# Kernel tuning notes

Hardware: AMD Instinct MI355X
Metric: run time of the kernel (lower is better)

The kernel has to match this reference:

```python
import jax, jax.numpy as jnp
import numpy as np


def _kernelize(data, projection_matrix):
    # FAVOR+ positive softmax features: ratio * h(x) * f(x @ P^T)
    # h(x) = exp(-||x||^2 / 2), f(u) = exp(u)
    d = data.shape[-1]
    r = projection_matrix.shape[0]
    data_norm = (d ** -0.25) * data                       # [n, d]
    ratio = r ** -0.5
    data_dash = jnp.einsum('id,rd->ir', data_norm, projection_matrix)  # [n, r]
    h = jnp.exp(-0.5 * jnp.sum(data_norm * data_norm, axis=-1, keepdims=True))  # [n, 1]
    return ratio * h * jnp.exp(data_dash)                 # [n, r]


def setup_inputs() -> dict:
    key = jax.random.key(0)
    k1, k2, k3, k4 = jax.random.split(key, 4)
    n, d, dv, r = 65536, 64, 64, 256
    q = jax.random.normal(k1, (n, d), dtype=jnp.float32)
    k = jax.random.normal(k2, (n, d), dtype=jnp.float32)
    v = jax.random.normal(k3, (n, dv), dtype=jnp.float32)
    projection_matrix = jax.random.normal(k4, (r, d), dtype=jnp.float32)
    return {"q": q, "k": k, "v": v, "projection_matrix": projection_matrix}


def reference(q, k, v, projection_matrix):
    q_hat = _kernelize(q, projection_matrix)              # [n, r]
    k_hat = _kernelize(k, projection_matrix)              # [n, r]
    z = k_hat.T @ v                                       # [r, dv]  (FAVOR associativity)
    w = q_hat @ z                                         # [n, dv]
    d_inv = 1.0 / jnp.sum(q_hat * jnp.sum(k_hat, axis=0), axis=1, keepdims=True)  # [n, 1]
    return d_inv * w
```

## Files before the change

kernel.cpp:

```cpp
#include <hip/hip_runtime.h>
#include <math.h>

typedef __attribute__((ext_vector_type(8))) short bf16x8;
typedef __attribute__((ext_vector_type(4))) float f32x4;

#define NROWS 65536
#define RFEAT 256
#define DDIM 64
#define NCOL 80
#define PARTN (RFEAT * NCOL)
#define NGROUP 16

#define SC 0.35355339059327373f
#define LNRATIO -2.772588722239781f

__device__ __forceinline__ unsigned short f2bf(float f) {
    union { float f; unsigned int u; } v; v.f = f;
    unsigned int r = v.u + 0x7FFFu + ((v.u >> 16) & 1u);
    return (unsigned short)(r >> 16);
}

__global__ void prep_pb_kernel(const float* __restrict__ P, unsigned short* __restrict__ Pb)
{
    const int t = threadIdx.x, l = t & 63, g = t >> 6;
    for (int f = g * 8; f < g * 8 + 8; f++) {
        const int kstep = f >> 4, nt = f & 15;
        const float* src = P + (nt * 16 + (l & 15)) * 64 + kstep * 32 + (l >> 4) * 8;
        bf16x8 frag;
        #pragma unroll
        for (int j = 0; j < 8; j++) frag[j] = (short)f2bf(SC * src[j]);
        *(bf16x8*)(Pb + f * 512 + l * 8) = frag;
    }
}

template<int LDP, bool TRANS>
__device__ __forceinline__ void phi_chunk(const float* __restrict__ X, int chunkBase,
                                          const unsigned short* __restrict__ Pb,
                                          unsigned short* phi_lds, float* rc)
{
    const int t = threadIdx.x, l = t & 63, w = t >> 6;
    if (t < 64) {
        const float4* xr = (const float4*)(X + (size_t)(chunkBase + t) * 64);
        float s0 = 0.f, s1 = 0.f;
        #pragma unroll
        for (int j = 0; j < 16; j += 2) {
            float4 a = xr[j];     s0 += a.x*a.x + a.y*a.y + a.z*a.z + a.w*a.w;
            float4 b = xr[j + 1]; s1 += b.x*b.x + b.y*b.y + b.z*b.z + b.w*b.w;
        }
        rc[t] = -0.5f * (SC * SC) * (s0 + s1) + LNRATIO;
    }
    const float* ar = X + (size_t)(chunkBase + 16 * w + (l & 15)) * 64 + (l >> 4) * 8;
    bf16x8 a0, a1;
    #pragma unroll
    for (int j = 0; j < 8; j++) a0[j] = (short)f2bf(ar[j]);
    #pragma unroll
    for (int j = 0; j < 8; j++) a1[j] = (short)f2bf(ar[32 + j]);
    __syncthreads();
    #pragma unroll
    for (int nt = 0; nt < 16; nt++) {
        bf16x8 b0 = *(const bf16x8*)(Pb + nt * 512 + l * 8);
        bf16x8 b1 = *(const bf16x8*)(Pb + (16 + nt) * 512 + l * 8);
        f32x4 acc = (f32x4){0.f, 0.f, 0.f, 0.f};
        acc = __builtin_amdgcn_mfma_f32_16x16x32_bf16(a0, b0, acc, 0, 0, 0);
        acc = __builtin_amdgcn_mfma_f32_16x16x32_bf16(a1, b1, acc, 0, 0, 0);
        const int col = nt * 16 + (l & 15);
        #pragma unroll
        for (int reg = 0; reg < 4; reg++) {
            const int rloc = 16 * w + (l >> 4) * 4 + reg;
            float phi = __expf(acc[reg] + rc[rloc]);
            if (TRANS) phi_lds[col * LDP + rloc] = f2bf(phi);
            else       phi_lds[rloc * LDP + col] = f2bf(phi);
        }
    }
    __syncthreads();
}

__global__ __launch_bounds__(256, 2)
void kv_fused_kernel(const float* __restrict__ Kp, const float* __restrict__ V,
                     const unsigned short* __restrict__ Pb,
                     float* __restrict__ partials, int chunksPerBlock)
{
    __shared__ unsigned short phi_lds[RFEAT * 72];
    __shared__ float rc[64];
    const int t = threadIdx.x, l = t & 63, w = t >> 6;

    f32x4 acc[4][5];
    #pragma unroll
    for (int mt = 0; mt < 4; mt++)
        #pragma unroll
        for (int nt = 0; nt < 5; nt++) acc[mt][nt] = (f32x4){0.f, 0.f, 0.f, 0.f};

    bf16x8 ones;
    #pragma unroll
    for (int j = 0; j < 8; j++) ones[j] = (short)(((l & 15) == 0) ? 0x3F80 : 0);

    const int base = blockIdx.x * chunksPerBlock * 64;
    for (int c = 0; c < chunksPerBlock; c++) {
        const int cb = base + c * 64;
        phi_chunk<72, true>(Kp, cb, Pb, phi_lds, rc);
        #pragma unroll
        for (int ks = 0; ks < 2; ks++) {
            bf16x8 af[4];
            #pragma unroll
            for (int mt = 0; mt < 4; mt++)
                af[mt] = *(const bf16x8*)(phi_lds + (64 * w + mt * 16 + (l & 15)) * 72
                                          + ks * 32 + (l >> 4) * 8);
            const int krow = cb + ks * 32 + (l >> 4) * 8;
            bf16x8 bf4[4];
            #pragma unroll
            for (int nt = 0; nt < 4; nt++) {
                const float* vp = V + (size_t)krow * 64 + nt * 16 + (l & 15);
                bf16x8 bb;
                #pragma unroll
                for (int j = 0; j < 8; j++) bb[j] = (short)f2bf(vp[j * 64]);
                bf4[nt] = bb;
            }
            #pragma unroll
            for (int mt = 0; mt < 4; mt++) {
                #pragma unroll
                for (int nt = 0; nt < 4; nt++)
                    acc[mt][nt] = __builtin_amdgcn_mfma_f32_16x16x32_bf16(af[mt], bf4[nt], acc[mt][nt], 0, 0, 0);
                acc[mt][4] = __builtin_amdgcn_mfma_f32_16x16x32_bf16(af[mt], ones, acc[mt][4], 0, 0, 0);
            }
        }
    }
    float* slot = partials + (size_t)blockIdx.x * PARTN;
    #pragma unroll
    for (int mt = 0; mt < 4; mt++)
        #pragma unroll
        for (int nt = 0; nt < 5; nt++)
            #pragma unroll
            for (int reg = 0; reg < 4; reg++)
                slot[(64 * w + mt * 16 + (l >> 4) * 4 + reg) * 80 + nt * 16 + (l & 15)] = acc[mt][nt][reg];
}

__global__ __launch_bounds__(256)
void reduce1_kernel(const float* __restrict__ partials, float* __restrict__ p2,
                    int slotsPerGroup)
{
    const int idx = blockIdx.x * 256 + threadIdx.x;
    const int g = blockIdx.y;
    const float* base = partials + (size_t)g * slotsPerGroup * PARTN + idx;
    float s0 = 0.f, s1 = 0.f, s2 = 0.f, s3 = 0.f;
    int b = 0;
    for (; b + 4 <= slotsPerGroup; b += 4) {
        s0 += base[(size_t)(b + 0) * PARTN];
        s1 += base[(size_t)(b + 1) * PARTN];
        s2 += base[(size_t)(b + 2) * PARTN];
        s3 += base[(size_t)(b + 3) * PARTN];
    }
    for (; b < slotsPerGroup; b++) s0 += base[(size_t)b * PARTN];
    p2[(size_t)g * PARTN + idx] = (s0 + s1) + (s2 + s3);
}

__global__ __launch_bounds__(256)
void reduce2_kernel(const float* __restrict__ p2, unsigned short* __restrict__ Zb, int ngroups)
{
    const int idx = blockIdx.x * 256 + threadIdx.x;
    float s = 0.f;
    for (int g = 0; g < ngroups; g++) s += p2[(size_t)g * PARTN + idx];
    const int m = idx / 80, n = idx - m * 80;
    Zb[((m >> 3) * 80 + n) * 8 + (m & 7)] = f2bf(s);
}

__global__ __launch_bounds__(256, 2)
void q_out_kernel(const float* __restrict__ Q, const unsigned short* __restrict__ Pb,
                  const unsigned short* __restrict__ Zb, float* __restrict__ out)
{
    __shared__ unsigned short phi_lds[64 * 272];
    __shared__ float rc[64];
    const int t = threadIdx.x, l = t & 63, w = t >> 6;
    const int base = blockIdx.x * 64;

    phi_chunk<272, false>(Q, base, Pb, phi_lds, rc);

    f32x4 acc[5];
    #pragma unroll
    for (int nt = 0; nt < 5; nt++) acc[nt] = (f32x4){0.f, 0.f, 0.f, 0.f};

    #pragma unroll
    for (int ks = 0; ks < 8; ks++) {
        bf16x8 a = *(const bf16x8*)(phi_lds + (16 * w + (l & 15)) * 272 + ks * 32 + (l >> 4) * 8);
        #pragma unroll
        for (int nt = 0; nt < 5; nt++) {
            bf16x8 b = *(const bf16x8*)(Zb + ((ks * 4 + (l >> 4)) * 80 + nt * 16 + (l & 15)) * 8);
            acc[nt] = __builtin_amdgcn_mfma_f32_16x16x32_bf16(a, b, acc[nt], 0, 0, 0);
        }
    }
    float inv[4];
    #pragma unroll
    for (int reg = 0; reg < 4; reg++) {
        float den = __shfl(acc[4][reg], (l & 48));
        inv[reg] = 1.0f / den;
    }
    const int row = base + 16 * w + (l >> 4) * 4;
    #pragma unroll
    for (int nt = 0; nt < 4; nt++)
        #pragma unroll
        for (int reg = 0; reg < 4; reg++)
            out[(size_t)(row + reg) * 64 + nt * 16 + (l & 15)] = acc[nt][reg] * inv[reg];
}

extern "C" void kernel_launch(void* const* d_in, const int* in_sizes, int n_in,
                              void* d_out, int out_size, void* d_ws, size_t ws_size,
                              hipStream_t stream) {
    const float* q = (const float*)d_in[0];
    const float* k = (const float*)d_in[1];
    const float* v = (const float*)d_in[2];
    const float* P = (const float*)d_in[3];
    float* out = (float*)d_out;

    unsigned short* Pb = (unsigned short*)d_ws;
    unsigned short* Zb = Pb + 32 * 512;
    float* p2 = (float*)((char*)d_ws + 32768 + 40960);
    float* partials = p2 + (size_t)NGROUP * PARTN;

    long fixedBytes = 32768 + 40960 + (long)NGROUP * PARTN * 4;
    long avail = ((long)ws_size - fixedBytes) / (long)(PARTN * 4);
    int NB = 512;
    while (NB > NGROUP && (long)NB > avail) NB >>= 1;
    int chunks = 1024 / NB;
    int ngroups = (NB >= NGROUP) ? NGROUP : NB;
    int spg = NB / ngroups;

    prep_pb_kernel<<<1, 256, 0, stream>>>(P, Pb);
    kv_fused_kernel<<<NB, 256, 0, stream>>>(k, v, Pb, partials, chunks);
    reduce1_kernel<<<dim3(80, ngroups), 256, 0, stream>>>(partials, p2, spg);
    reduce2_kernel<<<80, 256, 0, stream>>>(p2, Zb, ngroups);
    q_out_kernel<<<1024, 256, 0, stream>>>(q, Pb, Zb, out);
}
```

Measured before the change: 141.3 us.

## Pre-pack V into bf16 MFMA fragments and vectorize phi LDS stores

```diff
diff --git a/kernel.cpp b/kernel.cpp
--- a/kernel.cpp
+++ b/kernel.cpp
@@ -2,14 +2,20 @@
 #include <math.h>
 
 typedef __attribute__((ext_vector_type(8))) short bf16x8;
+typedef __attribute__((ext_vector_type(4))) short bf16x4;
 typedef __attribute__((ext_vector_type(4))) float f32x4;
 
 #define NROWS 65536
 #define RFEAT 256
-#define DDIM 64
 #define NCOL 80
 #define PARTN (RFEAT * NCOL)
 #define NGROUP 16
+
+#define OFF_PB 0
+#define OFF_ZB 32768
+#define OFF_P2 73728
+#define OFF_VB 1384448
+#define OFF_PARTIALS 9773056
 
 #define SC 0.35355339059327373f
 #define LNRATIO -2.772588722239781f
@@ -20,16 +26,44 @@
     return (unsigned short)(r >> 16);
 }
 
-__global__ void prep_pb_kernel(const float* __restrict__ P, unsigned short* __restrict__ Pb)
-{
-    const int t = threadIdx.x, l = t & 63, g = t >> 6;
-    for (int f = g * 8; f < g * 8 + 8; f++) {
-        const int kstep = f >> 4, nt = f & 15;
-        const float* src = P + (nt * 16 + (l & 15)) * 64 + kstep * 32 + (l >> 4) * 8;
-        bf16x8 frag;
-        #pragma unroll
-        for (int j = 0; j < 8; j++) frag[j] = (short)f2bf(SC * src[j]);
-        *(bf16x8*)(Pb + f * 512 + l * 8) = frag;
+__global__ __launch_bounds__(256)
+void prep_kernel(const float* __restrict__ V, const float* __restrict__ P,
+                 unsigned short* __restrict__ Vb, unsigned short* __restrict__ Pb)
+{
+    const int t = threadIdx.x;
+    if (blockIdx.x == 1024) {
+        const int l = t & 63, g = t >> 6;
+        for (int f = g * 8; f < g * 8 + 8; f++) {
+            const int kstep = f >> 4, nt = f & 15;
+            const float* src = P + (nt * 16 + (l & 15)) * 64 + kstep * 32 + (l >> 4) * 8;
+            bf16x8 frag;
+            #pragma unroll
+            for (int j = 0; j < 8; j++) frag[j] = (short)f2bf(SC * src[j]);
+            *(bf16x8*)(Pb + f * 512 + l * 8) = frag;
+        }
+        return;
+    }
+    __shared__ unsigned short vl[64 * 68];
+    const int row = t >> 2, c0 = (t & 3) * 16;
+    const float4* src = (const float4*)(V + ((size_t)blockIdx.x * 64 + row) * 64 + c0);
+    unsigned short* dst = vl + row * 68 + c0;
+    #pragma unroll
+    for (int jj = 0; jj < 4; jj++) {
+        float4 a = src[jj];
+        dst[4*jj+0] = f2bf(a.x); dst[4*jj+1] = f2bf(a.y);
+        dst[4*jj+2] = f2bf(a.z); dst[4*jj+3] = f2bf(a.w);
+    }
+    __syncthreads();
+    const int l = t & 63;
+    #pragma unroll
+    for (int h = 0; h < 2; h++) {
+        const int f = (t >> 6) * 2 + h;
+        const int ks = f >> 2, nt = f & 3;
+        const int kb = ks * 32 + (l >> 4) * 8, n = nt * 16 + (l & 15);
+        bf16x8 fr;
+        #pragma unroll
+        for (int j = 0; j < 8; j++) fr[j] = vl[(kb + j) * 68 + n];
+        *(bf16x8*)(Vb + (((size_t)blockIdx.x * 2 + ks) * 4 + nt) * 512 + l * 8) = fr;
     }
 }
 
@@ -64,19 +98,24 @@
         acc = __builtin_amdgcn_mfma_f32_16x16x32_bf16(a0, b0, acc, 0, 0, 0);
         acc = __builtin_amdgcn_mfma_f32_16x16x32_bf16(a1, b1, acc, 0, 0, 0);
         const int col = nt * 16 + (l & 15);
-        #pragma unroll
-        for (int reg = 0; reg < 4; reg++) {
-            const int rloc = 16 * w + (l >> 4) * 4 + reg;
-            float phi = __expf(acc[reg] + rc[rloc]);
-            if (TRANS) phi_lds[col * LDP + rloc] = f2bf(phi);
-            else       phi_lds[rloc * LDP + col] = f2bf(phi);
+        const int r0 = 16 * w + (l >> 4) * 4;
+        if (TRANS) {
+            bf16x4 pk;
+            #pragma unroll
+            for (int reg = 0; reg < 4; reg++)
+                pk[reg] = (short)f2bf(__expf(acc[reg] + rc[r0 + reg]));
+            *(bf16x4*)(phi_lds + col * LDP + r0) = pk;
+        } else {
+            #pragma unroll
+            for (int reg = 0; reg < 4; reg++)
+                phi_lds[(r0 + reg) * LDP + col] = f2bf(__expf(acc[reg] + rc[r0 + reg]));
         }
     }
     __syncthreads();
 }
 
 __global__ __launch_bounds__(256, 2)
-void kv_fused_kernel(const float* __restrict__ Kp, const float* __restrict__ V,
+void kv_fused_kernel(const float* __restrict__ Kp, const unsigned short* __restrict__ Vb,
                      const unsigned short* __restrict__ Pb,
                      float* __restrict__ partials, int chunksPerBlock)
 {
@@ -97,7 +136,16 @@
     const int base = blockIdx.x * chunksPerBlock * 64;
     for (int c = 0; c < chunksPerBlock; c++) {
         const int cb = base + c * 64;
+        bf16x8 vf[2][4];
+        const size_t k32 = (size_t)(cb >> 5);
+        #pragma unroll
+        for (int ks = 0; ks < 2; ks++)
+            #pragma unroll
+            for (int nt = 0; nt < 4; nt++)
+                vf[ks][nt] = *(const bf16x8*)(Vb + ((k32 + ks) * 4 + nt) * 512 + l * 8);
+
         phi_chunk<72, true>(Kp, cb, Pb, phi_lds, rc);
+
         #pragma unroll
         for (int ks = 0; ks < 2; ks++) {
             bf16x8 af[4];
@@ -105,21 +153,11 @@
             for (int mt = 0; mt < 4; mt++)
                 af[mt] = *(const bf16x8*)(phi_lds + (64 * w + mt * 16 + (l & 15)) * 72
                                           + ks * 32 + (l >> 4) * 8);
-            const int krow = cb + ks * 32 + (l >> 4) * 8;
-            bf16x8 bf4[4];
-            #pragma unroll
-            for (int nt = 0; nt < 4; nt++) {
-                const float* vp = V + (size_t)krow * 64 + nt * 16 + (l & 15);
-                bf16x8 bb;
-                #pragma unroll
-                for (int j = 0; j < 8; j++) bb[j] = (short)f2bf(vp[j * 64]);
-                bf4[nt] = bb;
-            }
             #pragma unroll
             for (int mt = 0; mt < 4; mt++) {
                 #pragma unroll
                 for (int nt = 0; nt < 4; nt++)
-                    acc[mt][nt] = __builtin_amdgcn_mfma_f32_16x16x32_bf16(af[mt], bf4[nt], acc[mt][nt], 0, 0, 0);
+                    acc[mt][nt] = __builtin_amdgcn_mfma_f32_16x16x32_bf16(af[mt], vf[ks][nt], acc[mt][nt], 0, 0, 0);
                 acc[mt][4] = __builtin_amdgcn_mfma_f32_16x16x32_bf16(af[mt], ones, acc[mt][4], 0, 0, 0);
             }
         }
@@ -167,12 +205,12 @@
 void q_out_kernel(const float* __restrict__ Q, const unsigned short* __restrict__ Pb,
                   const unsigned short* __restrict__ Zb, float* __restrict__ out)
 {
-    __shared__ unsigned short phi_lds[64 * 272];
+    __shared__ unsigned short phi_lds[64 * 280];
     __shared__ float rc[64];
     const int t = threadIdx.x, l = t & 63, w = t >> 6;
     const int base = blockIdx.x * 64;
 
-    phi_chunk<272, false>(Q, base, Pb, phi_lds, rc);
+    phi_chunk<280, false>(Q, base, Pb, phi_lds, rc);
 
     f32x4 acc[5];
     #pragma unroll
@@ -180,7 +218,7 @@
 
     #pragma unroll
     for (int ks = 0; ks < 8; ks++) {
-        bf16x8 a = *(const bf16x8*)(phi_lds + (16 * w + (l & 15)) * 272 + ks * 32 + (l >> 4) * 8);
+        bf16x8 a = *(const bf16x8*)(phi_lds + (16 * w + (l & 15)) * 280 + ks * 32 + (l >> 4) * 8);
         #pragma unroll
         for (int nt = 0; nt < 5; nt++) {
             bf16x8 b = *(const bf16x8*)(Zb + ((ks * 4 + (l >> 4)) * 80 + nt * 16 + (l & 15)) * 8);
@@ -210,21 +248,21 @@
     const float* P = (const float*)d_in[3];
     float* out = (float*)d_out;
 
-    unsigned short* Pb = (unsigned short*)d_ws;
-    unsigned short* Zb = Pb + 32 * 512;
-    float* p2 = (float*)((char*)d_ws + 32768 + 40960);
-    float* partials = p2 + (size_t)NGROUP * PARTN;
-
-    long fixedBytes = 32768 + 40960 + (long)NGROUP * PARTN * 4;
-    long avail = ((long)ws_size - fixedBytes) / (long)(PARTN * 4);
+    unsigned short* Pb = (unsigned short*)((char*)d_ws + OFF_PB);
+    unsigned short* Zb = (unsigned short*)((char*)d_ws + OFF_ZB);
+    float* p2          = (float*)((char*)d_ws + OFF_P2);
+    unsigned short* Vb = (unsigned short*)((char*)d_ws + OFF_VB);
+    float* partials    = (float*)((char*)d_ws + OFF_PARTIALS);
+
+    long avail = ((long)ws_size - OFF_PARTIALS) / (long)(PARTN * 4);
     int NB = 512;
     while (NB > NGROUP && (long)NB > avail) NB >>= 1;
     int chunks = 1024 / NB;
     int ngroups = (NB >= NGROUP) ? NGROUP : NB;
     int spg = NB / ngroups;
 
-    prep_pb_kernel<<<1, 256, 0, stream>>>(P, Pb);
-    kv_fused_kernel<<<NB, 256, 0, stream>>>(k, v, Pb, partials, chunks);
+    prep_kernel<<<1025, 256, 0, stream>>>(v, P, Vb, Pb);
+    kv_fused_kernel<<<NB, 256, 0, stream>>>(k, Vb, Pb, partials, chunks);
     reduce1_kernel<<<dim3(80, ngroups), 256, 0, stream>>>(partials, p2, spg);
     reduce2_kernel<<<80, 256, 0, stream>>>(p2, Zb, ngroups);
     q_out_kernel<<<1024, 256, 0, stream>>>(q, Pb, Zb, out);
```

Result: slower. 146.7 us (+3.8%).
